# Kernel optimization log

Measured on AMD Instinct MI355X. Metric: run time of the kernel, lower is better.

## Reference

```python
import jax, jax.numpy as jnp
import numpy as np

B, P, C, O = 64, 24564, 81, 20
THRESHOLD = 0.5
NEG_POS_RATIO = 3
ALPHA = 1.0


def cxcy_to_xy(c):
    return jnp.concatenate([c[..., :2] - c[..., 2:] / 2, c[..., :2] + c[..., 2:] / 2], -1)


def xy_to_cxcy(x):
    return jnp.concatenate([(x[..., :2] + x[..., 2:]) / 2, x[..., 2:] - x[..., :2]], -1)


def cxcy_to_gcxgcy(c, p):
    # SSD box encoding with variances (10, 5)
    return jnp.concatenate([(c[..., :2] - p[..., :2]) / (p[..., 2:] / 10.0),
                            jnp.log(c[..., 2:] / p[..., 2:]) * 5.0], -1)


def jaccard(a, b):
    # a: [O,4] xy, b: [P,4] xy -> [O,P]
    lt = jnp.maximum(a[:, None, :2], b[None, :, :2])
    rb = jnp.minimum(a[:, None, 2:], b[None, :, 2:])
    wh = jnp.clip(rb - lt, 0.0)
    inter = wh[..., 0] * wh[..., 1]
    area_a = (a[:, 2] - a[:, 0]) * (a[:, 3] - a[:, 1])
    area_b = (b[:, 2] - b[:, 0]) * (b[:, 3] - b[:, 1])
    union = area_a[:, None] + area_b[None, :] - inter
    return inter / union


def smooth_l1(x):
    ax = jnp.abs(x)
    return jnp.where(ax < 1.0, 0.5 * ax * ax, ax - 0.5)


def setup_inputs() -> dict:
    key = jax.random.key(0)
    k1, k2, k3, k4, k5, k6, k7 = jax.random.split(key, 7)
    predicted_locs = jax.random.normal(k1, (B, P, 4), jnp.float32)
    predicted_scores = jax.random.normal(k2, (B, P, C), jnp.float32)
    # valid ground-truth boxes in boundary (xy) coords
    cxy = jax.random.uniform(k3, (B, O, 2), jnp.float32, 0.2, 0.8)
    wh = jax.random.uniform(k4, (B, O, 2), jnp.float32, 0.05, 0.3)
    boxes = jnp.concatenate([cxy - wh / 2, cxy + wh / 2], -1)
    labels = jax.random.randint(k5, (B, O), 1, C).astype(jnp.int64)
    pxy = jax.random.uniform(k6, (P, 2), jnp.float32, 0.0, 1.0)
    pwh = jax.random.uniform(k7, (P, 2), jnp.float32, 0.05, 0.5)
    priors_cxcy = jnp.concatenate([pxy, pwh], -1)
    return {"predicted_locs": predicted_locs, "predicted_scores": predicted_scores,
            "boxes": boxes, "labels": labels, "priors_cxcy": priors_cxcy}


def reference(predicted_locs, predicted_scores, boxes, labels, priors_cxcy):
    priors_xy = cxcy_to_xy(priors_cxcy)
    n_priors = priors_cxcy.shape[0]

    def match(boxes_i, labels_i):
        overlap = jaccard(boxes_i, priors_xy)                 # [O,P]
        overlap_fp = overlap.max(axis=0)                      # [P]
        object_fp = overlap.argmax(axis=0)                    # [P]
        prior_fo = overlap.argmax(axis=1)                     # [O]
        object_fp = object_fp.at[prior_fo].set(jnp.arange(O))
        overlap_fp = overlap_fp.at[prior_fo].set(1.0)
        label_fp = labels_i[object_fp]
        label_fp = jnp.where(overlap_fp < THRESHOLD, 0, label_fp)
        true_locs_i = cxcy_to_gcxgcy(xy_to_cxcy(boxes_i[object_fp]), priors_cxcy)
        return true_locs_i, label_fp

    true_locs, true_classes = jax.vmap(match)(boxes, labels)  # [B,P,4], [B,P]

    positive = true_classes != 0                              # [B,P]
    n_positives = positive.sum(axis=1)                        # [B]
    total_pos = n_positives.sum()

    # confidence loss per prior (categorical CE, no reduction)
    logp = jax.nn.log_softmax(predicted_scores, axis=-1)
    conf_loss_all = -jnp.take_along_axis(logp, true_classes[..., None], axis=-1)[..., 0]  # [B,P]

    # location loss: smooth L1, mean over positive box elements
    posf = positive.astype(predicted_locs.dtype)
    loc_elems = smooth_l1(predicted_locs - true_locs) * posf[..., None]
    loc_loss = jnp.sum(loc_elems) / jnp.maximum(4.0 * total_pos.astype(loc_elems.dtype), 1.0)

    # hard negative mining
    conf_loss_pos_sum = jnp.sum(conf_loss_all * posf)
    conf_loss_neg = jnp.where(positive, 0.0, conf_loss_all)
    conf_loss_neg = -jnp.sort(-conf_loss_neg, axis=1)         # descending per row
    n_hard_neg = NEG_POS_RATIO * n_positives
    hard_mask = jnp.arange(n_priors)[None, :] < n_hard_neg[:, None]
    conf_loss_hard_neg_sum = jnp.sum(conf_loss_neg * hard_mask.astype(conf_loss_neg.dtype))

    conf_loss_matched = (conf_loss_hard_neg_sum + conf_loss_pos_sum) / jnp.maximum(
        total_pos.astype(conf_loss_all.dtype), 1.0)

    loss = jnp.where(total_pos > 0,
                     conf_loss_matched + ALPHA * loc_loss,
                     jnp.mean(conf_loss_all))
    return loss
```

## Files before the change

### kernel.cpp

```cpp
#include <hip/hip_runtime.h>
#include <math.h>

#define B_ 64
#define P_ 24564
#define C_ 81
#define O_ 20

__device__ __forceinline__ float iou_xy(float ax0, float ay0, float ax1, float ay1,
                                        float bx0, float by0, float bx1, float by1) {
#pragma clang fp contract(off)
    float lx = fmaxf(ax0, bx0), ly = fmaxf(ay0, by0);
    float rx = fminf(ax1, bx1), ry = fminf(ay1, by1);
    float w = fmaxf(rx - lx, 0.f), h = fmaxf(ry - ly, 0.f);
    float inter = w * h;
    float aa = (ax1 - ax0) * (ay1 - ay0);
    float ab = (bx1 - bx0) * (by1 - by0);
    return inter / (aa + ab - inter);
}

__device__ __forceinline__ float sl1(float d) {
#pragma clang fp contract(off)
    float a = fabsf(d);
    return a < 1.f ? 0.5f * a * a : a - 0.5f;
}

__global__ void k_prior(const float* __restrict__ boxes, const float* __restrict__ priors,
                        int* __restrict__ prior_fo, int* __restrict__ n_pos,
                        float* __restrict__ pos_sum, float* __restrict__ tot_sum,
                        float* __restrict__ loc_sum) {
#pragma clang fp contract(off)
    int o = blockIdx.x, b = blockIdx.y, t = threadIdx.x;
    if (o == 0 && t == 0) {
        n_pos[b] = 0; pos_sum[b] = 0.f; tot_sum[b] = 0.f; loc_sum[b] = 0.f;
    }
    const float* bx = boxes + ((size_t)b * O_ + o) * 4;
    float bx0 = bx[0], by0 = bx[1], bx1 = bx[2], by1 = bx[3];
    float best = -1.f;
    int bi = 0;
    for (int p = t; p < P_; p += 256) {
        float4 pr = ((const float4*)priors)[p];
        float px0 = pr.x - pr.z * 0.5f, py0 = pr.y - pr.w * 0.5f;
        float px1 = pr.x + pr.z * 0.5f, py1 = pr.y + pr.w * 0.5f;
        float v = iou_xy(bx0, by0, bx1, by1, px0, py0, px1, py1);
        if (v > best) { best = v; bi = p; }
    }
    __shared__ float sv[256];
    __shared__ int si[256];
    sv[t] = best; si[t] = bi;
    __syncthreads();
    for (int s = 128; s > 0; s >>= 1) {
        if (t < s) {
            float ov = sv[t + s]; int oi = si[t + s];
            if (ov > sv[t] || (ov == sv[t] && oi < si[t])) { sv[t] = ov; si[t] = oi; }
        }
        __syncthreads();
    }
    if (t == 0) prior_fo[b * O_ + o] = si[0];
}

__global__ void k_match(const float* __restrict__ boxes, const int* __restrict__ labels,
                        const float* __restrict__ priors, const float* __restrict__ plocs,
                        const int* __restrict__ prior_fo, unsigned char* __restrict__ true_class,
                        float* __restrict__ loc_sum, int* __restrict__ n_pos) {
#pragma clang fp contract(off)
    int b = blockIdx.y, t = threadIdx.x;
    int p = blockIdx.x * 256 + t;
    __shared__ float sb[O_][4];
    __shared__ float sc[O_][4];
    __shared__ int sl[O_];
    __shared__ int sf[O_];
    if (t < O_) {
        const float* bx = boxes + ((size_t)b * O_ + t) * 4;
        float x0 = bx[0], y0 = bx[1], x1 = bx[2], y1 = bx[3];
        sb[t][0] = x0; sb[t][1] = y0; sb[t][2] = x1; sb[t][3] = y1;
        sc[t][0] = (x0 + x1) * 0.5f; sc[t][1] = (y0 + y1) * 0.5f;
        sc[t][2] = x1 - x0;          sc[t][3] = y1 - y0;
        sl[t] = labels[b * O_ + t];
        sf[t] = prior_fo[b * O_ + t];
    }
    __syncthreads();
    float lsum = 0.f;
    int posc = 0;
    if (p < P_) {
        float4 pr = ((const float4*)priors)[p];
        float px0 = pr.x - pr.z * 0.5f, py0 = pr.y - pr.w * 0.5f;
        float px1 = pr.x + pr.z * 0.5f, py1 = pr.y + pr.w * 0.5f;
        float best = -1.f;
        int bi = 0;
        for (int o = 0; o < O_; o++) {
            float v = iou_xy(sb[o][0], sb[o][1], sb[o][2], sb[o][3], px0, py0, px1, py1);
            if (v > best) { best = v; bi = o; }
        }
        for (int o = 0; o < O_; o++)
            if (sf[o] == p) { bi = o; best = 1.0f; }
        int lab = (best < 0.5f) ? 0 : sl[bi];
        true_class[(size_t)b * P_ + p] = (unsigned char)lab;
        if (lab != 0) {
            posc = 1;
            float gx = (sc[bi][0] - pr.x) / (pr.z / 10.0f);
            float gy = (sc[bi][1] - pr.y) / (pr.w / 10.0f);
            float gw = logf(sc[bi][2] / pr.z) * 5.0f;
            float gh = logf(sc[bi][3] / pr.w) * 5.0f;
            float4 pl = ((const float4*)plocs)[(size_t)b * P_ + p];
            lsum = sl1(pl.x - gx) + sl1(pl.y - gy) + sl1(pl.z - gw) + sl1(pl.w - gh);
        }
    }
    for (int off = 32; off > 0; off >>= 1) {
        lsum += __shfl_down(lsum, off);
        posc += __shfl_down(posc, off);
    }
    __shared__ float wv[4];
    __shared__ int wc[4];
    int lane = t & 63, w = t >> 6;
    if (lane == 0) { wv[w] = lsum; wc[w] = posc; }
    __syncthreads();
    if (t == 0) {
        atomicAdd(&loc_sum[b], wv[0] + wv[1] + wv[2] + wv[3]);
        atomicAdd(&n_pos[b], wc[0] + wc[1] + wc[2] + wc[3]);
    }
}

__global__ __launch_bounds__(256) void k_conf(const float* __restrict__ scores,
                                              const unsigned char* __restrict__ true_class,
                                              float* __restrict__ conf_neg,
                                              float* __restrict__ pos_sum,
                                              float* __restrict__ tot_sum) {
    __shared__ float4 smem4[1296];
    float* smem = (float*)smem4;
    int b = blockIdx.y;
    int p0 = blockIdx.x * 64;
    int t = threadIdx.x, lane = t & 63, w = t >> 6;
    int rows = P_ - p0;
    if (rows > 64) rows = 64;
    int nf4 = rows * 81 / 4;
    const float4* gsrc = (const float4*)(scores + ((size_t)b * P_ + p0) * (size_t)C_);
    for (int i = t; i < nf4; i += 256) smem4[i] = gsrc[i];
    __syncthreads();

    int i = t >> 2;
    int q = t & 3;
    int p = p0 + i;
    bool active = (i < rows);
    int tcv = 0;
    if (q == 0 && active) tcv = true_class[(size_t)b * P_ + p];
    tcv = __shfl(tcv, lane & ~3, 64);

    float sum = 0.f, st = 0.f;
    if (active) {
        int base = q * 21;
        int cnt = (q == 3) ? 18 : 21;
        const float* r = smem + i * 81 + base;
        for (int j = 0; j < cnt; j++) {
            float v = r[j];
            sum += __expf(v);
            if (base + j == tcv) st = v;
        }
    }
    sum += __shfl_xor(sum, 1);
    sum += __shfl_xor(sum, 2);
    st += __shfl_xor(st, 1);
    st += __shfl_xor(st, 2);

    float ce = 0.f, posv = 0.f;
    if (active) {
        ce = __logf(sum) - st;
        if (tcv != 0) posv = ce;
        if (q == 0) conf_neg[(size_t)b * P_ + p] = (tcv == 0) ? ce : 0.f;
    }
    float tc_ = (q == 0) ? ce : 0.f;
    float pc_ = (q == 0) ? posv : 0.f;
    for (int off = 32; off > 0; off >>= 1) {
        tc_ += __shfl_down(tc_, off);
        pc_ += __shfl_down(pc_, off);
    }
    __shared__ float stt[4], spp[4];
    if (lane == 0) { stt[w] = tc_; spp[w] = pc_; }
    __syncthreads();
    if (t == 0) {
        atomicAdd(&tot_sum[b], stt[0] + stt[1] + stt[2] + stt[3]);
        atomicAdd(&pos_sum[b], spp[0] + spp[1] + spp[2] + spp[3]);
    }
}

__global__ __launch_bounds__(1024) void k_topk(const float* __restrict__ conf_neg,
                                               const int* __restrict__ n_pos,
                                               float* __restrict__ hard_sum) {
    int b = blockIdx.x, t = threadIdx.x, lane = t & 63, w = t >> 6;
    const float* row = conf_neg + (size_t)b * P_;
    unsigned vb[24];
#pragma unroll
    for (int i = 0; i < 24; i++) {
        int p = t + (i << 10);
        vb[i] = (p < P_) ? __float_as_uint(row[p]) : 0u;
    }
    int k = 3 * n_pos[b];
    __shared__ int cnts[32];
    __shared__ float ssum;
    __shared__ int scnt;
    if (k <= 0) {
        if (t == 0) hard_sum[b] = 0.f;
        return;
    }
    if (t < 32) cnts[t] = 0;
    if (t == 0) { ssum = 0.f; scnt = 0; }
    __syncthreads();
    unsigned lo = 0u, hi = 0x7F800000u;
    int pass = 0;
    while (lo < hi) {
        unsigned mid = lo + ((hi - lo) >> 1);
        int c = 0;
#pragma unroll
        for (int i = 0; i < 24; i++) c += (vb[i] > mid);
        for (int off = 32; off > 0; off >>= 1) c += __shfl_down(c, off);
        if (lane == 0) atomicAdd(&cnts[pass], c);
        __syncthreads();
        int cnt = cnts[pass];
        if (cnt < k) hi = mid; else lo = mid + 1;
        pass++;
    }
    float s = 0.f;
    int c = 0;
#pragma unroll
    for (int i = 0; i < 24; i++) {
        if (vb[i] > lo) { s += __uint_as_float(vb[i]); c++; }
    }
    for (int off = 32; off > 0; off >>= 1) {
        s += __shfl_down(s, off);
        c += __shfl_down(c, off);
    }
    if (lane == 0) { atomicAdd(&ssum, s); atomicAdd(&scnt, c); }
    __syncthreads();
    if (t == 0) hard_sum[b] = ssum + (float)(k - scnt) * __uint_as_float(lo);
}

__global__ void k_final(const int* __restrict__ n_pos, const float* __restrict__ pos_sum,
                        const float* __restrict__ tot_sum, const float* __restrict__ loc_sum,
                        const float* __restrict__ hard_sum, float* __restrict__ out) {
    int t = threadIdx.x;
    int np = n_pos[t];
    float ps = pos_sum[t], ts = tot_sum[t], ls = loc_sum[t], hs = hard_sum[t];
    for (int off = 32; off > 0; off >>= 1) {
        np += __shfl_down(np, off);
        ps += __shfl_down(ps, off);
        ts += __shfl_down(ts, off);
        ls += __shfl_down(ls, off);
        hs += __shfl_down(hs, off);
    }
    if (t == 0) {
        float tp = (float)np;
        float conf = (hs + ps) / fmaxf(tp, 1.f);
        float loc = ls / fmaxf(4.f * tp, 1.f);
        float mean = ts / ((float)B_ * (float)P_);
        out[0] = (np > 0) ? (conf + loc) : mean;
    }
}

extern "C" void kernel_launch(void* const* d_in, const int* in_sizes, int n_in,
                              void* d_out, int out_size, void* d_ws, size_t ws_size,
                              hipStream_t stream) {
    const float* plocs  = (const float*)d_in[0];
    const float* scores = (const float*)d_in[1];
    const float* boxes  = (const float*)d_in[2];
    const int*   labels = (const int*)d_in[3];
    const float* priors = (const float*)d_in[4];

    char* ws = (char*)d_ws;
    unsigned char* true_class = (unsigned char*)ws;
    float* conf_neg   = (float*)(ws + (size_t)B_ * P_);
    int*   prior_fo   = (int*)(ws + (size_t)B_ * P_ + (size_t)B_ * P_ * 4);
    int*   n_pos      = prior_fo + B_ * O_;
    float* pos_sum    = (float*)(n_pos + B_);
    float* tot_sum    = pos_sum + B_;
    float* loc_sum    = tot_sum + B_;
    float* hard_sum   = loc_sum + B_;

    k_prior<<<dim3(O_, B_), 256, 0, stream>>>(boxes, priors, prior_fo,
                                              n_pos, pos_sum, tot_sum, loc_sum);
    k_match<<<dim3((P_ + 255) / 256, B_), 256, 0, stream>>>(
        boxes, labels, priors, plocs, prior_fo, true_class, loc_sum, n_pos);
    k_conf<<<dim3((P_ + 63) / 64, B_), 256, 0, stream>>>(
        scores, true_class, conf_neg, pos_sum, tot_sum);
    k_topk<<<B_, 1024, 0, stream>>>(conf_neg, n_pos, hard_sum);
    k_final<<<1, 64, 0, stream>>>(n_pos, pos_sum, tot_sum, loc_sum, hard_sum, (float*)d_out);
}
```

Before: 907.5 us.

## Fuse prior matching into confidence kernel, dropping the true_class buffer

Merges the matching kernel into the confidence kernel. Each group of 4 lanes that shares a prior splits the 20 IoU computations between them and reduces the best match with shuffles. This removes one kernel launch and the write and re-read of the per-prior true_class byte array, and the box and label loads overlap with the score tile load. The cost is extra per-thread work and registers in the score-loading kernel, and a tie-break rule that now has to match the original lowest-index argmax.

Result: faster. 861.3 us (-5.1%).

```diff
diff --git a/kernel.cpp b/kernel.cpp
--- a/kernel.cpp
+++ b/kernel.cpp
@@ -58,75 +58,24 @@
     if (t == 0) prior_fo[b * O_ + o] = si[0];
 }
 
-__global__ void k_match(const float* __restrict__ boxes, const int* __restrict__ labels,
-                        const float* __restrict__ priors, const float* __restrict__ plocs,
-                        const int* __restrict__ prior_fo, unsigned char* __restrict__ true_class,
-                        float* __restrict__ loc_sum, int* __restrict__ n_pos) {
-#pragma clang fp contract(off)
-    int b = blockIdx.y, t = threadIdx.x;
-    int p = blockIdx.x * 256 + t;
+__global__ __launch_bounds__(256) void k_cm(const float* __restrict__ scores,
+                                            const float* __restrict__ boxes,
+                                            const int* __restrict__ labels,
+                                            const float* __restrict__ priors,
+                                            const float* __restrict__ plocs,
+                                            const int* __restrict__ prior_fo,
+                                            float* __restrict__ conf_neg,
+                                            float* __restrict__ pos_sum,
+                                            float* __restrict__ tot_sum,
+                                            float* __restrict__ loc_sum,
+                                            int* __restrict__ n_pos) {
+#pragma clang fp contract(off)
+    __shared__ float4 smem4[1296];
+    float* smem = (float*)smem4;
     __shared__ float sb[O_][4];
     __shared__ float sc[O_][4];
-    __shared__ int sl[O_];
+    __shared__ int sl_[O_];
     __shared__ int sf[O_];
-    if (t < O_) {
-        const float* bx = boxes + ((size_t)b * O_ + t) * 4;
-        float x0 = bx[0], y0 = bx[1], x1 = bx[2], y1 = bx[3];
-        sb[t][0] = x0; sb[t][1] = y0; sb[t][2] = x1; sb[t][3] = y1;
-        sc[t][0] = (x0 + x1) * 0.5f; sc[t][1] = (y0 + y1) * 0.5f;
-        sc[t][2] = x1 - x0;          sc[t][3] = y1 - y0;
-        sl[t] = labels[b * O_ + t];
-        sf[t] = prior_fo[b * O_ + t];
-    }
-    __syncthreads();
-    float lsum = 0.f;
-    int posc = 0;
-    if (p < P_) {
-        float4 pr = ((const float4*)priors)[p];
-        float px0 = pr.x - pr.z * 0.5f, py0 = pr.y - pr.w * 0.5f;
-        float px1 = pr.x + pr.z * 0.5f, py1 = pr.y + pr.w * 0.5f;
-        float best = -1.f;
-        int bi = 0;
-        for (int o = 0; o < O_; o++) {
-            float v = iou_xy(sb[o][0], sb[o][1], sb[o][2], sb[o][3], px0, py0, px1, py1);
-            if (v > best) { best = v; bi = o; }
-        }
-        for (int o = 0; o < O_; o++)
-            if (sf[o] == p) { bi = o; best = 1.0f; }
-        int lab = (best < 0.5f) ? 0 : sl[bi];
-        true_class[(size_t)b * P_ + p] = (unsigned char)lab;
-        if (lab != 0) {
-            posc = 1;
-            float gx = (sc[bi][0] - pr.x) / (pr.z / 10.0f);
-            float gy = (sc[bi][1] - pr.y) / (pr.w / 10.0f);
-            float gw = logf(sc[bi][2] / pr.z) * 5.0f;
-            float gh = logf(sc[bi][3] / pr.w) * 5.0f;
-            float4 pl = ((const float4*)plocs)[(size_t)b * P_ + p];
-            lsum = sl1(pl.x - gx) + sl1(pl.y - gy) + sl1(pl.z - gw) + sl1(pl.w - gh);
-        }
-    }
-    for (int off = 32; off > 0; off >>= 1) {
-        lsum += __shfl_down(lsum, off);
-        posc += __shfl_down(posc, off);
-    }
-    __shared__ float wv[4];
-    __shared__ int wc[4];
-    int lane = t & 63, w = t >> 6;
-    if (lane == 0) { wv[w] = lsum; wc[w] = posc; }
-    __syncthreads();
-    if (t == 0) {
-        atomicAdd(&loc_sum[b], wv[0] + wv[1] + wv[2] + wv[3]);
-        atomicAdd(&n_pos[b], wc[0] + wc[1] + wc[2] + wc[3]);
-    }
-}
-
-__global__ __launch_bounds__(256) void k_conf(const float* __restrict__ scores,
-                                              const unsigned char* __restrict__ true_class,
-                                              float* __restrict__ conf_neg,
-                                              float* __restrict__ pos_sum,
-                                              float* __restrict__ tot_sum) {
-    __shared__ float4 smem4[1296];
-    float* smem = (float*)smem4;
     int b = blockIdx.y;
     int p0 = blockIdx.x * 64;
     int t = threadIdx.x, lane = t & 63, w = t >> 6;
@@ -135,15 +84,55 @@
     int nf4 = rows * 81 / 4;
     const float4* gsrc = (const float4*)(scores + ((size_t)b * P_ + p0) * (size_t)C_);
     for (int i = t; i < nf4; i += 256) smem4[i] = gsrc[i];
+    if (t < O_) {
+        const float* bx = boxes + ((size_t)b * O_ + t) * 4;
+        float x0 = bx[0], y0 = bx[1], x1 = bx[2], y1 = bx[3];
+        sb[t][0] = x0; sb[t][1] = y0; sb[t][2] = x1; sb[t][3] = y1;
+        sc[t][0] = (x0 + x1) * 0.5f; sc[t][1] = (y0 + y1) * 0.5f;
+        sc[t][2] = x1 - x0;          sc[t][3] = y1 - y0;
+        sl_[t] = labels[b * O_ + t];
+        sf[t] = prior_fo[b * O_ + t];
+    }
     __syncthreads();
 
     int i = t >> 2;
     int q = t & 3;
     int p = p0 + i;
     bool active = (i < rows);
-    int tcv = 0;
-    if (q == 0 && active) tcv = true_class[(size_t)b * P_ + p];
-    tcv = __shfl(tcv, lane & ~3, 64);
+
+    int lab = 0;
+    float lsum = 0.f;
+    int posc = 0;
+    if (active) {
+        float4 pr = ((const float4*)priors)[p];
+        float px0 = pr.x - pr.z * 0.5f, py0 = pr.y - pr.w * 0.5f;
+        float px1 = pr.x + pr.z * 0.5f, py1 = pr.y + pr.w * 0.5f;
+        float best = -1.f;
+        int bi = 0x7fffffff;
+        for (int o = q; o < O_; o += 4) {
+            float v = iou_xy(sb[o][0], sb[o][1], sb[o][2], sb[o][3], px0, py0, px1, py1);
+            if (v > best || (v == best && o < bi)) { best = v; bi = o; }
+        }
+#pragma unroll
+        for (int off = 1; off <= 2; off <<= 1) {
+            float ov = __shfl_xor(best, off);
+            int oi = __shfl_xor(bi, off);
+            if (ov > best || (ov == best && oi < bi)) { best = ov; bi = oi; }
+        }
+        for (int o = 0; o < O_; o++)
+            if (sf[o] == p) { bi = o; best = 1.0f; }
+        lab = (best < 0.5f) ? 0 : sl_[bi];
+        if (lab != 0 && q == 0) {
+            posc = 1;
+            float gx = (sc[bi][0] - pr.x) / (pr.z / 10.0f);
+            float gy = (sc[bi][1] - pr.y) / (pr.w / 10.0f);
+            float gw = logf(sc[bi][2] / pr.z) * 5.0f;
+            float gh = logf(sc[bi][3] / pr.w) * 5.0f;
+            float4 pl = ((const float4*)plocs)[(size_t)b * P_ + p];
+            lsum = sl1(pl.x - gx) + sl1(pl.y - gy) + sl1(pl.z - gw) + sl1(pl.w - gh);
+        }
+    }
+    int tcv = lab;
 
     float sum = 0.f, st = 0.f;
     if (active) {
@@ -172,20 +161,28 @@
     for (int off = 32; off > 0; off >>= 1) {
         tc_ += __shfl_down(tc_, off);
         pc_ += __shfl_down(pc_, off);
-    }
-    __shared__ float stt[4], spp[4];
-    if (lane == 0) { stt[w] = tc_; spp[w] = pc_; }
+        lsum += __shfl_down(lsum, off);
+        posc += __shfl_down(posc, off);
+    }
+    __shared__ float stt[4], spp[4], sll[4];
+    __shared__ int snn[4];
+    if (lane == 0) { stt[w] = tc_; spp[w] = pc_; sll[w] = lsum; snn[w] = posc; }
     __syncthreads();
     if (t == 0) {
         atomicAdd(&tot_sum[b], stt[0] + stt[1] + stt[2] + stt[3]);
         atomicAdd(&pos_sum[b], spp[0] + spp[1] + spp[2] + spp[3]);
+        int n4 = snn[0] + snn[1] + snn[2] + snn[3];
+        if (n4 != 0) {
+            atomicAdd(&loc_sum[b], sll[0] + sll[1] + sll[2] + sll[3]);
+            atomicAdd(&n_pos[b], n4);
+        }
     }
 }
 
 __global__ __launch_bounds__(1024) void k_topk(const float* __restrict__ conf_neg,
                                                const int* __restrict__ n_pos,
                                                float* __restrict__ hard_sum) {
-    int b = blockIdx.x, t = threadIdx.x, lane = t & 63, w = t >> 6;
+    int b = blockIdx.x, t = threadIdx.x, lane = t & 63;
     const float* row = conf_neg + (size_t)b * P_;
     unsigned vb[24];
 #pragma unroll
@@ -265,9 +262,8 @@
     const float* priors = (const float*)d_in[4];
 
     char* ws = (char*)d_ws;
-    unsigned char* true_class = (unsigned char*)ws;
-    float* conf_neg   = (float*)(ws + (size_t)B_ * P_);
-    int*   prior_fo   = (int*)(ws + (size_t)B_ * P_ + (size_t)B_ * P_ * 4);
+    float* conf_neg   = (float*)ws;
+    int*   prior_fo   = (int*)(ws + (size_t)B_ * P_ * 4);
     int*   n_pos      = prior_fo + B_ * O_;
     float* pos_sum    = (float*)(n_pos + B_);
     float* tot_sum    = pos_sum + B_;
@@ -276,10 +272,9 @@
 
     k_prior<<<dim3(O_, B_), 256, 0, stream>>>(boxes, priors, prior_fo,
                                               n_pos, pos_sum, tot_sum, loc_sum);
-    k_match<<<dim3((P_ + 255) / 256, B_), 256, 0, stream>>>(
-        boxes, labels, priors, plocs, prior_fo, true_class, loc_sum, n_pos);
-    k_conf<<<dim3((P_ + 63) / 64, B_), 256, 0, stream>>>(
-        scores, true_class, conf_neg, pos_sum, tot_sum);
+    k_cm<<<dim3((P_ + 63) / 64, B_), 256, 0, stream>>>(
+        scores, boxes, labels, priors, plocs, prior_fo,
+        conf_neg, pos_sum, tot_sum, loc_sum, n_pos);
     k_topk<<<B_, 1024, 0, stream>>>(conf_neg, n_pos, hard_sum);
     k_final<<<1, 64, 0, stream>>>(n_pos, pos_sum, tot_sum, loc_sum, hard_sum, (float*)d_out);
 }
```
